# Optimization experiments

Hardware: AMD Instinct MI355X
Metric: run time of the kernel (lower is better)

## Reference

```python
import jax, jax.numpy as jnp
import numpy as np

SHIFTS = [1, 2, 4]  # matches init_kwargs 'shifts' (all in range 0 < s < channels)


def setup_inputs() -> dict:
    key = jax.random.key(0)
    k1, k2, k3 = jax.random.split(key, 3)
    B, H, L, D = 4, 1, 2048, 512
    factor = 4
    proj_in = 2 * len(SHIFTS) * D  # cli_mode='full' -> 2 components per shift
    x = jax.random.normal(k1, (B, H, L, D), dtype=jnp.float32)
    W = jax.random.normal(k2, (factor, D), dtype=jnp.float32) * 0.05
    # glorot-ish scale for the projection kernel
    proj_kernel = jax.random.normal(k3, (proj_in, D), dtype=jnp.float32) * (1.0 / np.sqrt(proj_in))
    proj_bias = jnp.zeros((D,), dtype=jnp.float32)
    return {"x": x, "W": W, "proj_kernel": proj_kernel, "proj_bias": proj_bias}


def reference(x, W, proj_kernel, proj_bias):
    # x: (B, H, L, D); W: (k, D) slot multivectors
    k, D = W.shape
    B, H, L, _ = x.shape
    # coarse[-1] treated as zeros; non-anchor slots source previous coarse vector
    coarse_prev = jnp.pad(x, ((0, 0), (0, 0), (1, 0), (0, 0)))[:, :, :-1, :]
    # src: (B, H, L, k, D) — slots 0..k-2 from coarse_prev, slot k-1 (anchor) from x
    src = jnp.concatenate(
        [jnp.repeat(coarse_prev[:, :, :, None, :], k - 1, axis=3),
         x[:, :, :, None, :]],
        axis=3,
    )
    W_b = W[None, None, None, :, :]  # (1,1,1,k,D)
    components = []
    for s in SHIFTS:
        src_s = jnp.roll(src, s, axis=-1)
        W_s_b = jnp.roll(W, s, axis=-1)[None, None, None, :, :]
        sw = src * W_s_b
        components.append(sw - W_b * src_s)        # wedge part
        components.append(jax.nn.silu(sw))          # inner part (full mode)
    g = jnp.concatenate(components, axis=-1)  # (B,H,L,k, 2*len(shifts)*D)
    fine = jnp.einsum('bhlkc,cd->bhlkd', g, proj_kernel) + proj_bias
    return fine.reshape(B, H, L * k, D)
```

## Files before the change

### kernel.cpp

```cpp
#include <hip/hip_runtime.h>
#include <cstdint>
#include <cstddef>

#define D_DIM 512
#define L_DIM 2048
#define KB_DIM 2048
#define NROWS_X 2049

typedef __bf16 bf16x8 __attribute__((ext_vector_type(8)));
typedef float  f32x4  __attribute__((ext_vector_type(4)));

__device__ __forceinline__ unsigned f2bf(float f) {
  unsigned u = __float_as_uint(f);
  u += 0x7FFF + ((u >> 16) & 1);
  return u >> 16;
}
__device__ __forceinline__ float bf2f(unsigned short u) {
  return __uint_as_float(((unsigned)u) << 16);
}
__device__ __forceinline__ void gld_lds16(const void* g, void* l) {
  __builtin_amdgcn_global_load_lds((const __attribute__((address_space(1))) void*)g,
                                   (__attribute__((address_space(3))) void*)l,
                                   16, 0, 0);
}

__global__ void convert_x(const float* __restrict__ x, unsigned short* __restrict__ XbfZ) {
  const int b = blockIdx.y;
  const int idx = blockIdx.x * 256 + threadIdx.x;
  if (idx >= NROWS_X * 128) return;
  const int rr = idx >> 7;
  const int c4 = idx & 127;
  uint2 p = {0u, 0u};
  if (rr > 0) {
    float4 v = reinterpret_cast<const float4*>(x)[((size_t)b * L_DIM + rr - 1) * 128 + c4];
    p.x = f2bf(v.x) | (f2bf(v.y) << 16);
    p.y = f2bf(v.z) | (f2bf(v.w) << 16);
  }
  reinterpret_cast<uint2*>(XbfZ)[((size_t)b * NROWS_X + rr) * 128 + c4] = p;
}

__global__ void build_B(const float* __restrict__ P, const float* __restrict__ W,
                        unsigned short* __restrict__ Ball) {
  const int bx = blockIdx.x;
  const int j = bx >> 6, dt = (bx >> 3) & 7, ct = bx & 7;
  const int t = threadIdx.x;
  const int d = dt * 64 + (t & 63);
  const int cbase = ct * 64 + (t >> 6) * 16;
  unsigned short bufd[16];
  unsigned short bufs[3][16];
  #pragma unroll
  for (int cc = 0; cc < 16; ++cc) {
    const int c = cbase + cc;
    float qd = 0.f;
    #pragma unroll
    for (int si = 0; si < 3; ++si) {
      const int s = 1 << si;
      const int cm = (c - s) & 511, cp = (c + s) & 511;
      qd += W[j * 512 + cm] * P[((size_t)(2 * si) * 512 + c) * 512 + d]
          - W[j * 512 + cp] * P[((size_t)(2 * si) * 512 + cp) * 512 + d];
      bufs[si][cc] = (unsigned short)f2bf(P[((size_t)(2 * si + 1) * 512 + c) * 512 + d]);
    }
    bufd[cc] = (unsigned short)f2bf(qd);
  }
  unsigned short* row = Ball + (size_t)(j * 512 + d) * KB_DIM;
  *reinterpret_cast<uint4*>(&row[cbase])     = *reinterpret_cast<uint4*>(&bufd[0]);
  *reinterpret_cast<uint4*>(&row[cbase + 8]) = *reinterpret_cast<uint4*>(&bufd[8]);
  #pragma unroll
  for (int si = 0; si < 3; ++si) {
    *reinterpret_cast<uint4*>(&row[512 + si * 512 + cbase])     = *reinterpret_cast<uint4*>(&bufs[si][0]);
    *reinterpret_cast<uint4*>(&row[512 + si * 512 + cbase + 8]) = *reinterpret_cast<uint4*>(&bufs[si][8]);
  }
}

__global__ __launch_bounds__(256, 2) void fused_gemm(
    const unsigned short* __restrict__ XbfZ, const unsigned short* __restrict__ Ball,
    const float* __restrict__ W, const float* __restrict__ bias,
    float* __restrict__ out) {
  __shared__ alignas(16) unsigned short Vt[2][4096];
  __shared__ alignas(16) unsigned short Bt[2][8192];
  __shared__ alignas(16) unsigned short At[128 * 40];
  __shared__ alignas(16) unsigned short Wr[3 * 512];

  const int tid = threadIdx.x;
  const int nt = blockIdx.x & 1;
  const int mt = blockIdx.x >> 1;
  const int j  = mt >> 6;
  const int b  = (mt >> 4) & 3;
  const int lt = mt & 15;
  const int l0 = lt * 128;
  const int n0 = nt * 256;
  const int base_l = l0 - ((j == 3) ? 0 : 1);

  #pragma unroll
  for (int i = 0; i < 6; ++i) {
    const int idx = tid + i * 256;
    const int si = idx >> 9, c = idx & 511, s = 1 << si;
    Wr[idx] = (unsigned short)f2bf(W[j * 512 + ((c - s) & 511)]);
  }

  const int lane = tid & 63, wv = tid >> 6;
  const int qv = (lane & 3) ^ ((lane >> 4) & 3);
  const int rsub = lane >> 2;
  const unsigned short* gA0 = XbfZ + ((size_t)(b * NROWS_X + 1 + base_l + (wv * 2) * 16 + rsub)) * 512 + qv * 8;
  const unsigned short* gA1 = gA0 + (size_t)16 * 512;
  const unsigned short* gB[4];
  #pragma unroll
  for (int pi = 0; pi < 4; ++pi)
    gB[pi] = Ball + (size_t)(j * 512 + n0 + (wv * 4 + pi) * 16 + rsub) * KB_DIM + qv * 8;
  const int vOff0 = wv * 1024 + lane * 8;
  const int bOff0 = wv * 2048 + lane * 8;

  const int am = tid >> 1;
  const int akh = (tid & 1) * 16;
  const int ch0 = (tid & 1) * 2;
  const int sswz = (am >> 2) & 3;
  unsigned short* aDst = &At[am * 40 + akh];

  const int l16 = lane & 15, quad = lane >> 4;
  const int wm = wv >> 1, wn = wv & 1;
  const int fsw = (l16 >> 2) & 3;
  const int aVoff = (wm * 64 + l16) * 32 + ((quad ^ fsw)) * 8;
  const int aSoff = (wm * 64 + l16) * 40 + quad * 8;
  const int bOffF = (wn * 128 + l16) * 32 + ((quad ^ fsw)) * 8;

  f32x4 acc[4][8];
  #pragma unroll
  for (int i = 0; i < 4; ++i)
    #pragma unroll
    for (int n = 0; n < 8; ++n)
      acc[i][n] = f32x4{0.f, 0.f, 0.f, 0.f};

  {
    gld_lds16(gA0, &Vt[0][vOff0]);
    gld_lds16(gA1, &Vt[0][vOff0 + 512]);
    #pragma unroll
    for (int pi = 0; pi < 4; ++pi)
      gld_lds16(gB[pi], &Bt[0][bOff0 + pi * 512]);
  }

  for (int it = 0; it < 64; ++it) {
    const int buf = it & 1;
    const int kk0 = it * 32;
    const int gi = kk0 >> 9;

    __syncthreads();

    if (it + 1 < 64) {
      const int nk = kk0 + 32;
      const int nv = nk & 511;
      gld_lds16(gA0 + nv, &Vt[buf ^ 1][vOff0]);
      gld_lds16(gA1 + nv, &Vt[buf ^ 1][vOff0 + 512]);
      #pragma unroll
      for (int pi = 0; pi < 4; ++pi)
        gld_lds16(gB[pi] + nk, &Bt[buf ^ 1][bOff0 + pi * 512]);
    }

    bf16x8 af[4], bfr[8];
    if (gi == 0) {
      #pragma unroll
      for (int mi = 0; mi < 4; ++mi) {
        uint4 r = *reinterpret_cast<const uint4*>(&Vt[buf][aVoff + mi * 512]);
        af[mi] = __builtin_bit_cast(bf16x8, r);
      }
    } else {
      const int si = gi - 1;
      const int ccbase = (kk0 & 511) + akh;
      uint4 v0 = *reinterpret_cast<const uint4*>(&Vt[buf][(am * 4 + ((ch0)     ^ sswz)) * 8]);
      uint4 v1 = *reinterpret_cast<const uint4*>(&Vt[buf][(am * 4 + ((ch0 + 1) ^ sswz)) * 8]);
      uint4 w0 = *reinterpret_cast<const uint4*>(&Wr[si * 512 + ccbase]);
      uint4 w1 = *reinterpret_cast<const uint4*>(&Wr[si * 512 + ccbase + 8]);
      union U { uint4 q[2]; unsigned short s[16]; };
      U va, wa; va.q[0] = v0; va.q[1] = v1; wa.q[0] = w0; wa.q[1] = w1;
      unsigned res[8];
      #pragma unroll
      for (int e = 0; e < 8; ++e) {
        float s0 = bf2f(va.s[2 * e])     * bf2f(wa.s[2 * e]);
        float s1 = bf2f(va.s[2 * e + 1]) * bf2f(wa.s[2 * e + 1]);
        float g0 = s0 * __builtin_amdgcn_rcpf(1.f + __expf(-s0));
        float g1 = s1 * __builtin_amdgcn_rcpf(1.f + __expf(-s1));
        res[e] = f2bf(g0) | (f2bf(g1) << 16);
      }
      uint4 o0 = {res[0], res[1], res[2], res[3]};
      uint4 o1 = {res[4], res[5], res[6], res[7]};
      *reinterpret_cast<uint4*>(aDst) = o0;
      *reinterpret_cast<uint4*>(aDst + 8) = o1;
      __syncthreads();
      #pragma unroll
      for (int mi = 0; mi < 4; ++mi) {
        uint4 r = *reinterpret_cast<const uint4*>(&At[aSoff + mi * 640]);
        af[mi] = __builtin_bit_cast(bf16x8, r);
      }
    }
    #pragma unroll
    for (int ni = 0; ni < 8; ++ni) {
      uint4 r = *reinterpret_cast<const uint4*>(&Bt[buf][bOffF + ni * 512]);
      bfr[ni] = __builtin_bit_cast(bf16x8, r);
    }
    #pragma unroll
    for (int mi = 0; mi < 4; ++mi)
      #pragma unroll
      for (int ni = 0; ni < 8; ++ni)
        acc[mi][ni] = __builtin_amdgcn_mfma_f32_16x16x32_bf16(af[mi], bfr[ni], acc[mi][ni], 0, 0, 0);
  }

  #pragma unroll
  for (int ni = 0; ni < 8; ++ni) {
    const int d = n0 + wn * 128 + ni * 16 + l16;
    const float bv = bias[d];
    #pragma unroll
    for (int mi = 0; mi < 4; ++mi) {
      const int lrow = l0 + wm * 64 + mi * 16 + quad * 4;
      #pragma unroll
      for (int rg = 0; rg < 4; ++rg) {
        out[((size_t)(b * L_DIM + lrow + rg) * 4 + j) * D_DIM + d] = acc[mi][ni][rg] + bv;
      }
    }
  }
}

extern "C" void kernel_launch(void* const* d_in, const int* in_sizes, int n_in,
                              void* d_out, int out_size, void* d_ws, size_t ws_size,
                              hipStream_t stream) {
  const float* x    = (const float*)d_in[0];
  const float* W    = (const float*)d_in[1];
  const float* P    = (const float*)d_in[2];
  const float* bias = (const float*)d_in[3];
  float* out = (float*)d_out;

  unsigned short* XbfZ = (unsigned short*)d_ws;
  unsigned short* Ball = XbfZ + (size_t)4 * NROWS_X * 512;

  convert_x<<<dim3(1025, 4), 256, 0, stream>>>(x, XbfZ);
  build_B<<<256, 256, 0, stream>>>(P, W, Ball);
  fused_gemm<<<512, 256, 0, stream>>>(XbfZ, Ball, W, bias, out);
}
```

Before: 201.6 us.

## Materialize SiLU operand in separate pass and use plain bf16 GEMM with smaller tiles

Instead of computing the SiLU inner-product operand inside the GEMM loop through an extra LDS stage and barrier, a new kernel precomputes the SiLU-transformed activations into a workspace matrix. A simpler GEMM then streams A from either the converted x rows or this precomputed matrix, using 128x128 tiles and 1024 blocks instead of 128x256 tiles and 512 blocks. This removes per-iteration elementwise work and an extra sync from the GEMM, at the cost of an extra kernel launch and about 96 MB of additional global traffic to write and reread the SiLU matrix. It falls back to the old fused kernel when the workspace is too small.

```diff
diff --git a/kernel.cpp b/kernel.cpp
--- a/kernel.cpp
+++ b/kernel.cpp
@@ -5,7 +5,9 @@
 #define D_DIM 512
 #define L_DIM 2048
 #define KB_DIM 2048
+#define KS_DIM 1536
 #define NROWS_X 2049
+#define M_TOT 32768
 
 typedef __bf16 bf16x8 __attribute__((ext_vector_type(8)));
 typedef float  f32x4  __attribute__((ext_vector_type(4)));
@@ -40,7 +42,16 @@
 }
 
 __global__ void build_B(const float* __restrict__ P, const float* __restrict__ W,
-                        unsigned short* __restrict__ Ball) {
+                        unsigned short* __restrict__ Ball,
+                        unsigned short* __restrict__ Wtab, int buildWtab) {
+  if (buildWtab && blockIdx.x == 0) {
+    for (int i = threadIdx.x; i < 6144; i += 256) {
+      const int c = i & 511; const int rest = i >> 9;
+      const int si = rest % 3; const int jj = rest / 3;
+      Wtab[(jj * 3 + si) * 512 + c] =
+          (unsigned short)f2bf(W[jj * 512 + ((c - (1 << si)) & 511)]);
+    }
+  }
   const int bx = blockIdx.x;
   const int j = bx >> 6, dt = (bx >> 3) & 7, ct = bx & 7;
   const int t = threadIdx.x;
@@ -69,6 +80,127 @@
   for (int si = 0; si < 3; ++si) {
     *reinterpret_cast<uint4*>(&row[512 + si * 512 + cbase])     = *reinterpret_cast<uint4*>(&bufs[si][0]);
     *reinterpret_cast<uint4*>(&row[512 + si * 512 + cbase + 8]) = *reinterpret_cast<uint4*>(&bufs[si][8]);
+  }
+}
+
+__global__ void gs_gen(const unsigned short* __restrict__ XbfZ,
+                       const unsigned short* __restrict__ Wtab,
+                       unsigned short* __restrict__ GS) {
+  const int m0 = blockIdx.x * 4;
+  const int j = m0 >> 13, b = (m0 >> 11) & 3, lbase = m0 & 2047;
+  const int r = threadIdx.x >> 6, lane = threadIdx.x & 63;
+  const int l = lbase + r;
+  const size_t vrow = (size_t)b * NROWS_X + l + (j == 3);
+  union U { uint4 q; unsigned short s[8]; };
+  U va;
+  va.q = *reinterpret_cast<const uint4*>(XbfZ + vrow * 512 + lane * 8);
+  unsigned short* o = GS + (size_t)(m0 + r) * KS_DIM + lane * 8;
+  #pragma unroll
+  for (int si = 0; si < 3; ++si) {
+    U wa;
+    wa.q = *reinterpret_cast<const uint4*>(Wtab + (j * 3 + si) * 512 + lane * 8);
+    unsigned res[4];
+    #pragma unroll
+    for (int e = 0; e < 4; ++e) {
+      float s0 = bf2f(va.s[2 * e])     * bf2f(wa.s[2 * e]);
+      float s1 = bf2f(va.s[2 * e + 1]) * bf2f(wa.s[2 * e + 1]);
+      float g0 = s0 * __builtin_amdgcn_rcpf(1.f + __expf(-s0));
+      float g1 = s1 * __builtin_amdgcn_rcpf(1.f + __expf(-s1));
+      res[e] = f2bf(g0) | (f2bf(g1) << 16);
+    }
+    uint4 ov = {res[0], res[1], res[2], res[3]};
+    *reinterpret_cast<uint4*>(o + si * 512) = ov;
+  }
+}
+
+__global__ __launch_bounds__(256) void gemm_main(
+    const unsigned short* __restrict__ XbfZ, const unsigned short* __restrict__ GS,
+    const unsigned short* __restrict__ Ball, const float* __restrict__ bias,
+    float* __restrict__ out) {
+  __shared__ alignas(16) unsigned short At[2][4096];
+  __shared__ alignas(16) unsigned short Bt[2][4096];
+
+  const int tid = threadIdx.x;
+  const int bx = blockIdx.x;
+  const int nt = bx >> 8;
+  const int mt = bx & 255;
+  const int j  = mt >> 6;
+  const int b  = (mt >> 4) & 3;
+  const int l0 = (mt & 15) * 128;
+  const int n0 = nt * 128;
+
+  const int rA = tid >> 2;
+  const int qA = (tid & 3) ^ ((rA >> 2) & 3);
+  const unsigned short* srcAd0 = XbfZ + (size_t)(b * NROWS_X + l0 + (j == 3) + rA) * 512 + qA * 8;
+  const unsigned short* srcAd1 = srcAd0 + (size_t)64 * 512;
+  const size_t mbase = (size_t)((j * 4 + b) * L_DIM + l0);
+  const unsigned short* srcAs0 = GS + (mbase + rA) * KS_DIM + qA * 8;
+  const unsigned short* srcAs1 = srcAs0 + (size_t)64 * KS_DIM;
+  const unsigned short* srcB0 = Ball + (size_t)(j * 512 + n0 + rA) * KB_DIM + qA * 8;
+  const unsigned short* srcB1 = srcB0 + (size_t)64 * KB_DIM;
+
+  const int lane = tid & 63, wv = tid >> 6;
+  const int wm = wv >> 1, wn = wv & 1;
+  const int l16 = lane & 15, quad = lane >> 4;
+  const int qf = quad ^ ((l16 >> 2) & 3);
+  const int aBase = (wm * 64 + l16) * 32 + qf * 8;
+  const int bBase = (wn * 64 + l16) * 32 + qf * 8;
+
+  f32x4 acc[4][4];
+  #pragma unroll
+  for (int i = 0; i < 4; ++i)
+    #pragma unroll
+    for (int n = 0; n < 4; ++n)
+      acc[i][n] = f32x4{0.f, 0.f, 0.f, 0.f};
+
+  gld_lds16(srcAd0, &At[0][tid * 8]);
+  gld_lds16(srcAd1, &At[0][(tid + 256) * 8]);
+  gld_lds16(srcB0,  &Bt[0][tid * 8]);
+  gld_lds16(srcB1,  &Bt[0][(tid + 256) * 8]);
+
+  for (int it = 0; it < 64; ++it) {
+    const int buf = it & 1;
+    __syncthreads();
+    if (it + 1 < 64) {
+      const int nx = it + 1, nb = buf ^ 1;
+      const unsigned short *a0, *a1;
+      if (nx < 16) { a0 = srcAd0 + nx * 32; a1 = srcAd1 + nx * 32; }
+      else { const int o = (nx - 16) * 32; a0 = srcAs0 + o; a1 = srcAs1 + o; }
+      gld_lds16(a0, &At[nb][tid * 8]);
+      gld_lds16(a1, &At[nb][(tid + 256) * 8]);
+      gld_lds16(srcB0 + nx * 32, &Bt[nb][tid * 8]);
+      gld_lds16(srcB1 + nx * 32, &Bt[nb][(tid + 256) * 8]);
+    }
+    bf16x8 af[4], bfr[4];
+    #pragma unroll
+    for (int mi = 0; mi < 4; ++mi) {
+      uint4 rr = *reinterpret_cast<const uint4*>(&At[buf][aBase + mi * 512]);
+      af[mi] = __builtin_bit_cast(bf16x8, rr);
+    }
+    #pragma unroll
+    for (int ni = 0; ni < 4; ++ni) {
+      uint4 rr = *reinterpret_cast<const uint4*>(&Bt[buf][bBase + ni * 512]);
+      bfr[ni] = __builtin_bit_cast(bf16x8, rr);
+    }
+    #pragma unroll
+    for (int mi = 0; mi < 4; ++mi)
+      #pragma unroll
+      for (int ni = 0; ni < 4; ++ni)
+        acc[mi][ni] = __builtin_amdgcn_mfma_f32_16x16x32_bf16(af[mi], bfr[ni], acc[mi][ni], 0, 0, 0);
+  }
+
+  #pragma unroll
+  for (int ni = 0; ni < 4; ++ni) {
+    const int d = n0 + wn * 64 + ni * 16 + l16;
+    const float bv = bias[d];
+    #pragma unroll
+    for (int mi = 0; mi < 4; ++mi) {
+      const int lrow = l0 + wm * 64 + mi * 16 + quad * 4;
+      #pragma unroll
+      for (int rg = 0; rg < 4; ++rg) {
+        out[((size_t)(b * L_DIM + lrow + rg) * 4 + j) * D_DIM + d] = acc[mi][ni][rg] + bv;
+      }
+    }
   }
 }
 
@@ -229,8 +361,19 @@
 
   unsigned short* XbfZ = (unsigned short*)d_ws;
   unsigned short* Ball = XbfZ + (size_t)4 * NROWS_X * 512;
+  unsigned short* Wtab = Ball + (size_t)4 * 512 * KB_DIM;
+  unsigned short* GS   = Wtab + 6144;
+  const size_t need_bytes =
+      ((size_t)4 * NROWS_X * 512 + (size_t)4 * 512 * KB_DIM + 6144 +
+       (size_t)M_TOT * KS_DIM) * 2;
+  const bool primary = ws_size >= need_bytes;
 
   convert_x<<<dim3(1025, 4), 256, 0, stream>>>(x, XbfZ);
-  build_B<<<256, 256, 0, stream>>>(P, W, Ball);
-  fused_gemm<<<512, 256, 0, stream>>>(XbfZ, Ball, W, bias, out);
-}
+  build_B<<<256, 256, 0, stream>>>(P, W, Ball, Wtab, primary ? 1 : 0);
+  if (primary) {
+    gs_gen<<<8192, 256, 0, stream>>>(XbfZ, Wtab, GS);
+    gemm_main<<<1024, 256, 0, stream>>>(XbfZ, GS, Ball, bias, out);
+  } else {
+    fused_gemm<<<512, 256, 0, stream>>>(XbfZ, Ball, W, bias, out);
+  }
+}
```

Result: no change. 199.4 us (-1.1%).

## Shrink GEMM tile to 128x128 and apply SiLU in registers on A fragments

Applied to the files above, without the earlier changes.

The fused GEMM changes from 128x256 tiles with 512 blocks to 128x128 tiles with 1024 blocks. Each wave now owns 32 rows across all 128 columns, and occupancy is raised to 4 blocks per SM. The SiLU-gated A operand is computed directly in MFMA fragment registers from the swizzled LDS V tile, using fp32 W weights. This removes the staging At buffer and the extra __syncthreads on SiLU iterations. The cost is less reuse of each B fragment per block and duplicated SiLU work across the two column tiles.

```diff
diff --git a/kernel.cpp b/kernel.cpp
--- a/kernel.cpp
+++ b/kernel.cpp
@@ -14,9 +14,6 @@
   unsigned u = __float_as_uint(f);
   u += 0x7FFF + ((u >> 16) & 1);
   return u >> 16;
-}
-__device__ __forceinline__ float bf2f(unsigned short u) {
-  return __uint_as_float(((unsigned)u) << 16);
 }
 __device__ __forceinline__ void gld_lds16(const void* g, void* l) {
   __builtin_amdgcn_global_load_lds((const __attribute__((address_space(1))) void*)g,
@@ -72,144 +69,119 @@
   }
 }
 
-__global__ __launch_bounds__(256, 2) void fused_gemm(
+__global__ __launch_bounds__(256, 4) void gemm_main(
     const unsigned short* __restrict__ XbfZ, const unsigned short* __restrict__ Ball,
     const float* __restrict__ W, const float* __restrict__ bias,
     float* __restrict__ out) {
   __shared__ alignas(16) unsigned short Vt[2][4096];
-  __shared__ alignas(16) unsigned short Bt[2][8192];
-  __shared__ alignas(16) unsigned short At[128 * 40];
-  __shared__ alignas(16) unsigned short Wr[3 * 512];
+  __shared__ alignas(16) unsigned short Btl[2][4096];
+  __shared__ alignas(16) float Wr[1536];
 
   const int tid = threadIdx.x;
-  const int nt = blockIdx.x & 1;
-  const int mt = blockIdx.x >> 1;
+  const int bx = blockIdx.x;
+  const int nt = bx >> 8;
+  const int mt = bx & 255;
   const int j  = mt >> 6;
   const int b  = (mt >> 4) & 3;
-  const int lt = mt & 15;
-  const int l0 = lt * 128;
-  const int n0 = nt * 256;
-  const int base_l = l0 - ((j == 3) ? 0 : 1);
+  const int l0 = (mt & 15) * 128;
+  const int n0 = nt * 128;
 
   #pragma unroll
   for (int i = 0; i < 6; ++i) {
     const int idx = tid + i * 256;
-    const int si = idx >> 9, c = idx & 511, s = 1 << si;
-    Wr[idx] = (unsigned short)f2bf(W[j * 512 + ((c - s) & 511)]);
-  }
+    const int si = idx >> 9, c = idx & 511;
+    Wr[idx] = W[j * 512 + ((c - (1 << si)) & 511)];
+  }
+
+  const int row1   = 2 * (tid >> 3) + ((tid >> 2) & 1);
+  const int chunk1 = (tid & 3) ^ ((tid >> 3) & 3);
+  const unsigned short* srcV =
+      XbfZ + ((size_t)b * NROWS_X + l0 + (j == 3) + row1) * 512 + chunk1 * 8;
+  const unsigned short* srcB =
+      Ball + ((size_t)(j * 512 + n0 + row1)) * KB_DIM + chunk1 * 8;
 
   const int lane = tid & 63, wv = tid >> 6;
-  const int qv = (lane & 3) ^ ((lane >> 4) & 3);
-  const int rsub = lane >> 2;
-  const unsigned short* gA0 = XbfZ + ((size_t)(b * NROWS_X + 1 + base_l + (wv * 2) * 16 + rsub)) * 512 + qv * 8;
-  const unsigned short* gA1 = gA0 + (size_t)16 * 512;
-  const unsigned short* gB[4];
-  #pragma unroll
-  for (int pi = 0; pi < 4; ++pi)
-    gB[pi] = Ball + (size_t)(j * 512 + n0 + (wv * 4 + pi) * 16 + rsub) * KB_DIM + qv * 8;
-  const int vOff0 = wv * 1024 + lane * 8;
-  const int bOff0 = wv * 2048 + lane * 8;
-
-  const int am = tid >> 1;
-  const int akh = (tid & 1) * 16;
-  const int ch0 = (tid & 1) * 2;
-  const int sswz = (am >> 2) & 3;
-  unsigned short* aDst = &At[am * 40 + akh];
-
   const int l16 = lane & 15, quad = lane >> 4;
-  const int wm = wv >> 1, wn = wv & 1;
-  const int fsw = (l16 >> 2) & 3;
-  const int aVoff = (wm * 64 + l16) * 32 + ((quad ^ fsw)) * 8;
-  const int aSoff = (wm * 64 + l16) * 40 + quad * 8;
-  const int bOffF = (wn * 128 + l16) * 32 + ((quad ^ fsw)) * 8;
-
-  f32x4 acc[4][8];
-  #pragma unroll
-  for (int i = 0; i < 4; ++i)
+  const int posf  = ((quad ^ ((l16 >> 1) & 3)) + 4 * (l16 & 1)) * 8;
+  const int aOff0 = (wv * 16 + (l16 >> 1)) * 64 + posf;
+  const int bOff0 = (l16 >> 1) * 64 + posf;
+  const int wOff  = quad * 8;
+
+  f32x4 acc[2][8];
+  #pragma unroll
+  for (int i = 0; i < 2; ++i)
     #pragma unroll
     for (int n = 0; n < 8; ++n)
       acc[i][n] = f32x4{0.f, 0.f, 0.f, 0.f};
 
-  {
-    gld_lds16(gA0, &Vt[0][vOff0]);
-    gld_lds16(gA1, &Vt[0][vOff0 + 512]);
-    #pragma unroll
-    for (int pi = 0; pi < 4; ++pi)
-      gld_lds16(gB[pi], &Bt[0][bOff0 + pi * 512]);
-  }
+  gld_lds16(srcV, &Vt[0][tid * 8]);
+  gld_lds16(srcV + (size_t)64 * 512, &Vt[0][(tid + 256) * 8]);
+  gld_lds16(srcB, &Btl[0][tid * 8]);
+  gld_lds16(srcB + (size_t)64 * KB_DIM, &Btl[0][(tid + 256) * 8]);
 
   for (int it = 0; it < 64; ++it) {
     const int buf = it & 1;
-    const int kk0 = it * 32;
-    const int gi = kk0 >> 9;
-
     __syncthreads();
-
     if (it + 1 < 64) {
-      const int nk = kk0 + 32;
-      const int nv = nk & 511;
-      gld_lds16(gA0 + nv, &Vt[buf ^ 1][vOff0]);
-      gld_lds16(gA1 + nv, &Vt[buf ^ 1][vOff0 + 512]);
+      const int kv = ((it + 1) * 32) & 511;
+      const int kb = (it + 1) * 32;
+      gld_lds16(srcV + kv, &Vt[buf ^ 1][tid * 8]);
+      gld_lds16(srcV + (size_t)64 * 512 + kv, &Vt[buf ^ 1][(tid + 256) * 8]);
+      gld_lds16(srcB + kb, &Btl[buf ^ 1][tid * 8]);
+      gld_lds16(srcB + (size_t)64 * KB_DIM + kb, &Btl[buf ^ 1][(tid + 256) * 8]);
+    }
+
+    bf16x8 af[2];
+    if (it < 16) {
       #pragma unroll
-      for (int pi = 0; pi < 4; ++pi)
-        gld_lds16(gB[pi] + nk, &Bt[buf ^ 1][bOff0 + pi * 512]);
-    }
-
-    bf16x8 af[4], bfr[8];
-    if (gi == 0) {
-      #pragma unroll
-      for (int mi = 0; mi < 4; ++mi) {
-        uint4 r = *reinterpret_cast<const uint4*>(&Vt[buf][aVoff + mi * 512]);
-        af[mi] = __builtin_bit_cast(bf16x8, r);
+      for (int mi = 0; mi < 2; ++mi) {
+        uint4 vr = *reinterpret_cast<const uint4*>(&Vt[buf][aOff0 + mi * 512]);
+        af[mi] = __builtin_bit_cast(bf16x8, vr);
       }
     } else {
-      const int si = gi - 1;
-      const int ccbase = (kk0 & 511) + akh;
-      uint4 v0 = *reinterpret_cast<const uint4*>(&Vt[buf][(am * 4 + ((ch0)     ^ sswz)) * 8]);
-      uint4 v1 = *reinterpret_cast<const uint4*>(&Vt[buf][(am * 4 + ((ch0 + 1) ^ sswz)) * 8]);
-      uint4 w0 = *reinterpret_cast<const uint4*>(&Wr[si * 512 + ccbase]);
-      uint4 w1 = *reinterpret_cast<const uint4*>(&Wr[si * 512 + ccbase + 8]);
-      union U { uint4 q[2]; unsigned short s[16]; };
-      U va, wa; va.q[0] = v0; va.q[1] = v1; wa.q[0] = w0; wa.q[1] = w1;
-      unsigned res[8];
+      const int si = (it >> 4) - 1;
+      const int kwin = (it * 32) & 511;
+      const float* wp = &Wr[si * 512 + kwin + wOff];
+      const float4 wa = *reinterpret_cast<const float4*>(wp);
+      const float4 wb = *reinterpret_cast<const float4*>(wp + 4);
+      const float wreg[8] = {wa.x, wa.y, wa.z, wa.w, wb.x, wb.y, wb.z, wb.w};
       #pragma unroll
-      for (int e = 0; e < 8; ++e) {
-        float s0 = bf2f(va.s[2 * e])     * bf2f(wa.s[2 * e]);
-        float s1 = bf2f(va.s[2 * e + 1]) * bf2f(wa.s[2 * e + 1]);
-        float g0 = s0 * __builtin_amdgcn_rcpf(1.f + __expf(-s0));
-        float g1 = s1 * __builtin_amdgcn_rcpf(1.f + __expf(-s1));
-        res[e] = f2bf(g0) | (f2bf(g1) << 16);
+      for (int mi = 0; mi < 2; ++mi) {
+        uint4 vr = *reinterpret_cast<const uint4*>(&Vt[buf][aOff0 + mi * 512]);
+        unsigned vv[4] = {vr.x, vr.y, vr.z, vr.w};
+        unsigned pk[4];
+        #pragma unroll
+        for (int e = 0; e < 4; ++e) {
+          const float vlo = __uint_as_float(vv[e] << 16);
+          const float vhi = __uint_as_float(vv[e] & 0xFFFF0000u);
+          const float xlo = vlo * wreg[2 * e];
+          const float xhi = vhi * wreg[2 * e + 1];
+          const float glo = xlo * __builtin_amdgcn_rcpf(1.f + __expf(-xlo));
+          const float ghi = xhi * __builtin_amdgcn_rcpf(1.f + __expf(-xhi));
+          pk[e] = __builtin_amdgcn_perm(__float_as_uint(ghi) + 0x8000u,
+                                        __float_as_uint(glo) + 0x8000u, 0x07060302u);
+        }
+        uint4 pr = {pk[0], pk[1], pk[2], pk[3]};
+        af[mi] = __builtin_bit_cast(bf16x8, pr);
       }
-      uint4 o0 = {res[0], res[1], res[2], res[3]};
-      uint4 o1 = {res[4], res[5], res[6], res[7]};
-      *reinterpret_cast<uint4*>(aDst) = o0;
-      *reinterpret_cast<uint4*>(aDst + 8) = o1;
-      __syncthreads();
-      #pragma unroll
-      for (int mi = 0; mi < 4; ++mi) {
-        uint4 r = *reinterpret_cast<const uint4*>(&At[aSoff + mi * 640]);
-        af[mi] = __builtin_bit_cast(bf16x8, r);
-      }
-    }
+    }
+
     #pragma unroll
     for (int ni = 0; ni < 8; ++ni) {
-      uint4 r = *reinterpret_cast<const uint4*>(&Bt[buf][bOffF + ni * 512]);
-      bfr[ni] = __builtin_bit_cast(bf16x8, r);
-    }
-    #pragma unroll
-    for (int mi = 0; mi < 4; ++mi)
-      #pragma unroll
-      for (int ni = 0; ni < 8; ++ni)
-        acc[mi][ni] = __builtin_amdgcn_mfma_f32_16x16x32_bf16(af[mi], bfr[ni], acc[mi][ni], 0, 0, 0);
+      uint4 br = *reinterpret_cast<const uint4*>(&Btl[buf][bOff0 + ni * 512]);
+      bf16x8 bf = __builtin_bit_cast(bf16x8, br);
+      acc[0][ni] = __builtin_amdgcn_mfma_f32_16x16x32_bf16(af[0], bf, acc[0][ni], 0, 0, 0);
+      acc[1][ni] = __builtin_amdgcn_mfma_f32_16x16x32_bf16(af[1], bf, acc[1][ni], 0, 0, 0);
+    }
   }
 
   #pragma unroll
   for (int ni = 0; ni < 8; ++ni) {
-    const int d = n0 + wn * 128 + ni * 16 + l16;
+    const int d = n0 + ni * 16 + l16;
     const float bv = bias[d];
     #pragma unroll
-    for (int mi = 0; mi < 4; ++mi) {
-      const int lrow = l0 + wm * 64 + mi * 16 + quad * 4;
+    for (int mi = 0; mi < 2; ++mi) {
+      const int lrow = l0 + wv * 32 + mi * 16 + quad * 4;
       #pragma unroll
       for (int rg = 0; rg < 4; ++rg) {
         out[((size_t)(b * L_DIM + lrow + rg) * 4 + j) * D_DIM + d] = acc[mi][ni][rg] + bv;
@@ -232,5 +204,5 @@
 
   convert_x<<<dim3(1025, 4), 256, 0, stream>>>(x, XbfZ);
   build_B<<<256, 256, 0, stream>>>(P, W, Ball);
-  fused_gemm<<<512, 256, 0, stream>>>(XbfZ, Ball, W, bias, out);
-}
+  gemm_main<<<1024, 256, 0, stream>>>(XbfZ, Ball, W, bias, out);
+}
```

New measurement: 208.6 us. +3.5%, slower.
